# Optimization experiments

Measured on AMD Instinct MI355X. Metric: run time of the kernel, lower is better.

## Reference

```python
import jax, jax.numpy as jnp
import numpy as np

HEADS = 8


def setup_inputs() -> dict:
    key = jax.random.key(0)
    ks = jax.random.split(key, 9)
    B, C, W, H = 8, 512, 32, 32
    dk = C // HEADS
    return {
        "x": jax.random.normal(ks[0], (B, C, W, H), dtype=jnp.float32),
        "wq": jax.random.normal(ks[1], (C, C), dtype=jnp.float32) * (1.0 / np.sqrt(C)),
        "bq": jax.random.normal(ks[2], (C,), dtype=jnp.float32) * 0.02,
        "wk": jax.random.normal(ks[3], (C, C), dtype=jnp.float32) * (1.0 / np.sqrt(C)),
        "bk": jax.random.normal(ks[4], (C,), dtype=jnp.float32) * 0.02,
        "wv": jax.random.normal(ks[5], (C, C), dtype=jnp.float32) * (1.0 / np.sqrt(C)),
        "bv": jax.random.normal(ks[6], (C,), dtype=jnp.float32) * 0.02,
        "rel_h": jax.random.normal(ks[7], (1, HEADS, dk, 1, H), dtype=jnp.float32),
        "rel_w": jax.random.normal(ks[8], (1, HEADS, dk, W, 1), dtype=jnp.float32),
    }


def reference(x, wq, bq, wk, bk, wv, bv, rel_h, rel_w):
    B, C, W, H = x.shape
    dk = C // HEADS
    N = W * H

    def proj(w, b):
        # 1x1 conv == per-pixel linear map over channels
        y = jnp.einsum('bchw,oc->bohw', x, w) + b[None, :, None, None]
        return y.reshape(B, HEADS, dk, N)

    q = proj(wq, bq)  # [B, h, dk, N]
    k = proj(wk, bk)
    v = proj(wv, bv)

    # content-content: q^T k -> [B, h, N, N]
    content_content = jnp.einsum('bhdn,bhdm->bhnm', q, k)

    # content-position: (rel_h + rel_w) -> [1, h, dk, W, H] -> [h, dk, N]
    pos = (rel_h + rel_w).reshape(HEADS, dk, N)
    # matmul(pos^T, q): [h, N, dk] @ [B, h, dk, N] -> [B, h, N, N]
    content_position = jnp.einsum('hdn,bhdm->bhnm', pos, q)

    energy = content_content + content_position
    attention = jax.nn.softmax(energy, axis=-1)  # softmax over last dim

    # out = v @ attention^T : [B, h, dk, N]
    out = jnp.einsum('bhdn,bhmn->bhdm', v, attention)
    return out.reshape(B, C, W, H)
```

## Files before the change

kernel.cpp:

```cpp
#include <hip/hip_runtime.h>

#define NPIX 1024
#define CC   512
#define DK   64
#define LOG2E 1.4426950408889634f

typedef __attribute__((ext_vector_type(8)))  short s16x8;
typedef __attribute__((ext_vector_type(8)))  _Float16 f16x8;
typedef __attribute__((ext_vector_type(16))) float f32x16;

union U4 { uint4 u; s16x8 v; };
union U4H { uint4 u; f16x8 v; };

__device__ __forceinline__ ushort f2bf(float f) {
  uint u = __float_as_uint(f);
  uint r = (u + 0x7fffu + ((u >> 16) & 1u)) >> 16;
  return (ushort)r;
}
__device__ __forceinline__ float bf2f(ushort h) { return __uint_as_float(((uint)h) << 16); }
__device__ __forceinline__ ushort f2h(float f) {
  union { _Float16 h; ushort u; } c;
  c.h = (_Float16)f;
  return c.u;
}
__device__ __forceinline__ float h2f(ushort u) {
  union { ushort u; _Float16 h; } c;
  c.u = u;
  return (float)c.h;
}

__device__ __forceinline__ uint cvtpk(float a, float b) {
  uint r;
  asm("v_cvt_pk_bf16_f32 %0, %1, %2" : "=v"(r) : "v"(a), "v"(b));
  return r;
}
__device__ __forceinline__ float fmax3(float a, float b, float c) {
  float d;
  asm("v_max3_f32 %0, %1, %2, %3" : "=v"(d) : "v"(a), "v"(b), "v"(c));
  return d;
}
__device__ __forceinline__ float exp2raw(float x) {
  float r;
  asm("v_exp_f32 %0, %1" : "=v"(r) : "v"(x));
  return r;
}

__device__ __forceinline__ f32x16 mfma32(s16x8 a, s16x8 b, f32x16 c) {
  return __builtin_amdgcn_mfma_f32_32x32x16_bf16(a, b, c, 0, 0, 0);
}
__device__ __forceinline__ f32x16 mfma32h(f16x8 a, f16x8 b, f32x16 c) {
  return __builtin_amdgcn_mfma_f32_32x32x16_f16(a, b, c, 0, 0, 0);
}

__device__ __forceinline__ void gl16(const void* g, void* l) {
  __builtin_amdgcn_global_load_lds(
      (const __attribute__((address_space(1))) void*)g,
      (__attribute__((address_space(3))) void*)l, 16, 0, 0);
}

__global__ void pos_kernel(const float* __restrict__ rel_h,
                           const float* __restrict__ rel_w,
                           ushort* __restrict__ posH, ushort* __restrict__ posL) {
  int t = blockIdx.x * 256 + threadIdx.x;
  int g = t & 7;
  int n = (t >> 3) & (NPIX - 1);
  int h = t >> 13;
  int xw = n >> 5, yh = n & 31;
  ushort hbuf[8], lbuf[8];
#pragma unroll
  for (int j = 0; j < 8; ++j) {
    int d = g * 8 + j;
    float v = rel_h[(h * 64 + d) * 32 + yh] + rel_w[(h * 64 + d) * 32 + xw];
    ushort hi = f2h(v);
    hbuf[j] = hi;
    lbuf[j] = f2h(v - h2f(hi));
  }
  size_t base = ((size_t)(h * NPIX + n)) * 64 + g * 8;
  *(uint4*)&posH[base] = *(uint4*)hbuf;
  *(uint4*)&posL[base] = *(uint4*)lbuf;
}

__global__ __launch_bounds__(256) void cvt_w_kernel(
    const float* __restrict__ wq, const float* __restrict__ wk,
    const float* __restrict__ wv,
    ushort* __restrict__ Wh, ushort* __restrict__ Wl) {
  int lin8 = blockIdx.x * 256 + threadIdx.x;
  int p = lin8 >> 15;
  int o = (lin8 & 32767) >> 6;
  int co = lin8 & 63;
  const float* Wsrc = (p == 0) ? wq : (p == 1) ? wk : wv;
  const float* src = &Wsrc[o * CC + co * 8];
  float4 f0 = *(const float4*)src;
  float4 f1 = *(const float4*)(src + 4);
  float f[8] = {f0.x, f0.y, f0.z, f0.w, f1.x, f1.y, f1.z, f1.w};
  ushort h8[8], l8[8];
#pragma unroll
  for (int j = 0; j < 8; ++j) {
    float sv = f[j] * 64.0f;
    ushort hi = f2h(sv);
    h8[j] = hi;
    l8[j] = f2h(sv - h2f(hi));
  }
  size_t dst = ((size_t)(p * CC + o)) * CC + co * 8;
  *(uint4*)&Wh[dst] = *(uint4*)h8;
  *(uint4*)&Wl[dst] = *(uint4*)l8;
}

__global__ __launch_bounds__(256) void cvt_x_kernel(
    const float* __restrict__ x, ushort* __restrict__ Xh) {
  int t = blockIdx.x * 256 + threadIdx.x;
  int nl = t & (NPIX - 1);
  int rest = t >> 10;
  int co = rest & 63;
  int b = rest >> 6;
  ushort h8[8];
#pragma unroll
  for (int j = 0; j < 8; ++j) {
    float v = x[(((size_t)(b * CC + co * 8 + j)) << 10) + nl];
    h8[j] = f2h(v);
  }
  size_t dst = (((size_t)(b * NPIX + nl)) << 9) + co * 8;
  *(uint4*)&Xh[dst] = *(uint4*)h8;
}

__global__ __launch_bounds__(256, 2) void proj_kernel(
    const ushort* __restrict__ Xh, const ushort* __restrict__ Wh,
    const ushort* __restrict__ Wl,
    const float* __restrict__ bq, const float* __restrict__ bk,
    const float* __restrict__ bv,
    ushort* __restrict__ KQh, ushort* __restrict__ KQl,
    ushort* __restrict__ Vb) {
  __shared__ __align__(16) ushort sW[128 * 128];
  __shared__ __align__(16) ushort sX[128 * 64];

  int tid = threadIdx.x;
  int lane = tid & 63;
  int w = tid >> 6;
  int col = lane & 31;
  int half = lane >> 5;
  int srow = lane >> 4;
  int sslot = lane & 15;

  int z = blockIdx.z;
  int b = z / 3, p = z % 3;
  const float* bias = (p == 0) ? bq : (p == 1) ? bk : bv;

  int n0 = blockIdx.x * 128;
  int o0 = blockIdx.y * 128;
  int wo = w >> 1;
  int wn = w & 1;

  f32x16 acc[2][2];
#pragma unroll
  for (int i = 0; i < 2; ++i)
#pragma unroll
    for (int j = 0; j < 2; ++j)
#pragma unroll
      for (int r = 0; r < 16; ++r) acc[i][j][r] = 0.f;

#pragma unroll 1
  for (int c0 = 0; c0 < CC; c0 += 64) {
#pragma unroll
    for (int i = 0; i < 8; ++i) {
      int rbase = (i * 4 + w) * 4;
      int row = rbase + srow;
      int j = sslot ^ (row & 15);
      int jc = j & 7;
      const ushort* src = (j < 8 || p == 2) ? Wh : Wl;
      size_t g = ((size_t)(p * CC + o0 + row)) * CC + c0 + jc * 8;
      gl16(src + g, (char*)sW + rbase * 256);
    }
#pragma unroll
    for (int i = 0; i < 4; ++i) {
      int rbase = i * 32 + w * 8;
      int row = rbase + (lane >> 3);
      int jc = (lane & 7) ^ (row & 7);
      size_t g = ((size_t)(b * NPIX + n0 + row)) * CC + c0 + jc * 8;
      gl16(Xh + g, (char*)sX + rbase * 128);
    }
    __syncthreads();

#pragma unroll
    for (int s = 0; s < 4; ++s) {
      if (p < 2) {
        f16x8 xa[2], wh_[2], wl_[2];
#pragma unroll
        for (int mt = 0; mt < 2; ++mt) {
          int row = wn * 64 + mt * 32 + col;
          int slot = ((s * 2 + half) ^ (row & 7)) << 4;
          xa[mt] = *(const f16x8*)((const char*)sX + row * 128 + slot);
        }
#pragma unroll
        for (int ct = 0; ct < 2; ++ct) {
          int row = wo * 64 + ct * 32 + col;
          int sh = ((s * 2 + half) ^ (row & 15)) << 4;
          int sl = ((8 + s * 2 + half) ^ (row & 15)) << 4;
          wh_[ct] = *(const f16x8*)((const char*)sW + row * 256 + sh);
          wl_[ct] = *(const f16x8*)((const char*)sW + row * 256 + sl);
        }
#pragma unroll
        for (int mt = 0; mt < 2; ++mt)
#pragma unroll
          for (int ct = 0; ct < 2; ++ct) {
            acc[mt][ct] = mfma32h(xa[mt], wh_[ct], acc[mt][ct]);
            acc[mt][ct] = mfma32h(xa[mt], wl_[ct], acc[mt][ct]);
          }
      } else {
        f16x8 wa[2], xb[2];
#pragma unroll
        for (int mt = 0; mt < 2; ++mt) {
          int row = wo * 64 + mt * 32 + col;
          int sh = ((s * 2 + half) ^ (row & 15)) << 4;
          wa[mt] = *(const f16x8*)((const char*)sW + row * 256 + sh);
        }
#pragma unroll
        for (int ct = 0; ct < 2; ++ct) {
          int row = wn * 64 + ct * 32 + col;
          int slot = ((s * 2 + half) ^ (row & 7)) << 4;
          xb[ct] = *(const f16x8*)((const char*)sX + row * 128 + slot);
        }
#pragma unroll
        for (int mt = 0; mt < 2; ++mt)
#pragma unroll
          for (int ct = 0; ct < 2; ++ct)
            acc[mt][ct] = mfma32h(wa[mt], xb[ct], acc[mt][ct]);
      }
    }
    __syncthreads();
  }

  const float INV64 = 0.015625f;
  if (p < 2) {
    float qscale = (p == 0) ? LOG2E : 1.0f;
#pragma unroll
    for (int ct = 0; ct < 2; ++ct) {
      int o = o0 + wo * 64 + ct * 32 + col;
      int bh = b * 8 + (o >> 6);
      int kk = ((p == 0) ? 64 : 0) + (o & 63);
      float bias_v = bias[o];
#pragma unroll
      for (int mt = 0; mt < 2; ++mt) {
        int nbase = n0 + wn * 64 + mt * 32;
#pragma unroll
        for (int r = 0; r < 16; ++r) {
          int n = nbase + (r & 3) + 8 * (r >> 2) + 4 * half;
          float v = (acc[mt][ct][r] * INV64 + bias_v) * qscale;
          ushort hi = f2h(v);
          size_t addr = (((size_t)bh << 10) + n) * 128 + kk;
          KQh[addr] = hi;
          if (p == 0) KQl[addr] = f2h(v - h2f(hi));
        }
      }
    }
  } else {
#pragma unroll
    for (int ct = 0; ct < 2; ++ct) {
      int n = n0 + wn * 64 + ct * 32 + col;
#pragma unroll
      for (int mt = 0; mt < 2; ++mt) {
        int obase = o0 + wo * 64 + mt * 32;
#pragma unroll
        for (int r = 0; r < 16; ++r) {
          int o = obase + (r & 3) + 8 * (r >> 2) + 4 * half;
          int bh = b * 8 + (o >> 6);
          int d = o & 63;
          float v = acc[mt][ct][r] * INV64 + bias[o];
          Vb[(((size_t)(bh * 64 + d)) << 10) + n] = f2bf(v);
        }
      }
    }
  }
}

__global__ __launch_bounds__(256, 2) void attn_kernel(
    const ushort* __restrict__ KQh, const ushort* __restrict__ KQl,
    const ushort* __restrict__ posH, const ushort* __restrict__ posL,
    const ushort* __restrict__ Vb, float* __restrict__ out) {
  __shared__ __align__(16) ushort sKh[128 * 128];
  __shared__ __align__(16) ushort sV[64 * 128];

  int tid = threadIdx.x;
  int lane = tid & 63;
  int w = tid >> 6;

  int bid = blockIdx.x;
  int wg = (bid & 7) * 64 + (bid >> 3);
  int bh = wg >> 3;
  int qb = wg & 7;
  int h = bh & 7;

  int col = lane & 31;
  int half = lane >> 5;
  int q0 = qb * 128 + w * 32;
  int q = q0 + col;

  uint4 bqh[8], bql[8];
  {
    const ushort* rowQh = KQh + ((size_t)bh * NPIX + q) * 128;
    const ushort* rowQl = KQl + ((size_t)bh * NPIX + q) * 128;
#pragma unroll
    for (int s = 0; s < 4; ++s) {
      int off = 64 + s * 16 + half * 8;
      bqh[s] = *(const uint4*)(rowQh + off);
      bql[s] = *(const uint4*)(rowQl + off);
    }
    const ushort* rowPh = posH + ((size_t)(h * NPIX + q)) * 64;
    const ushort* rowPl = posL + ((size_t)(h * NPIX + q)) * 64;
#pragma unroll
    for (int s = 4; s < 8; ++s) {
      int off = (s - 4) * 16 + half * 8;
      bqh[s] = *(const uint4*)(rowPh + off);
      bql[s] = *(const uint4*)(rowPl + off);
    }
  }

  f32x16 oacc[2];
#pragma unroll
  for (int t = 0; t < 2; ++t)
#pragma unroll
    for (int r = 0; r < 16; ++r) oacc[t][r] = 0.f;
  float m_ = -1e30f, l_ = 0.f;

  int srow = lane >> 4;
  int sslot = lane & 15;

#pragma unroll 1
  for (int k0 = 0; k0 < NPIX; k0 += 128) {
#pragma unroll
    for (int i = 0; i < 8; ++i) {
      int row = w * 32 + i * 4 + srow;
      size_t goff = ((size_t)bh * NPIX + k0 + row) * 128 + ((sslot ^ (row & 15)) << 3);
      char* ldst = (char*)sKh + (w * 32 + i * 4) * 256;
      gl16(KQh + goff, ldst);
    }
#pragma unroll
    for (int i = 0; i < 4; ++i) {
      int d = w * 16 + i * 4 + srow;
      size_t goff = ((size_t)(bh * 64 + d)) * NPIX + k0 + ((sslot ^ (d & 15)) << 3);
      char* ldst = (char*)sV + (w * 16 + i * 4) * 256;
      gl16(Vb + goff, ldst);
    }
    __syncthreads();

    f32x16 sa[4];
#pragma unroll
    for (int t = 0; t < 4; ++t)
#pragma unroll
      for (int r = 0; r < 16; ++r) sa[t][r] = 0.f;

    __builtin_amdgcn_s_setprio(1);
#pragma unroll
    for (int s = 0; s < 8; ++s) {
      U4H ubh, ubl;
      ubh.u = bqh[s];
      ubl.u = bql[s];
#pragma unroll
      for (int t = 0; t < 4; ++t) {
        int row = t * 32 + col;
        int slot = ((s * 2 + half) ^ (row & 15)) << 4;
        const f16x8 ah = *(const f16x8*)((const char*)sKh + row * 256 + slot);
        sa[t] = mfma32h(ah, ubh.v, sa[t]);
        sa[t] = mfma32h(ah, ubl.v, sa[t]);
      }
    }
    __builtin_amdgcn_s_setprio(0);

    float mx = -1e30f;
#pragma unroll
    for (int t = 0; t < 4; ++t)
#pragma unroll
      for (int r = 0; r < 16; r += 2) mx = fmax3(mx, sa[t][r], sa[t][r + 1]);
    mx = fmaxf(mx, __shfl_xor(mx, 32));
    if (!__all(mx - m_ <= 11.54f)) {
      float mn = fmaxf(m_, mx);
      float sc = exp2raw(m_ - mn);
      l_ *= sc;
#pragma unroll
      for (int t = 0; t < 2; ++t)
#pragma unroll
        for (int r = 0; r < 16; ++r) oacc[t][r] *= sc;
      m_ = mn;
    }
    float ssum = 0.f;
#pragma unroll
    for (int t = 0; t < 4; ++t)
#pragma unroll
      for (int r = 0; r < 16; ++r) {
        float pv = exp2raw(sa[t][r] - m_);
        sa[t][r] = pv;
        ssum += pv;
      }
    ssum += __shfl_xor(ssum, 32);
    l_ += ssum;

#pragma unroll
    for (int t = 0; t < 4; ++t) {
      uint ua[4], ub[4], xa[4], xb[4];
#pragma unroll
      for (int g = 0; g < 4; ++g) {
        ua[g] = cvtpk(sa[t][4 * g + 0], sa[t][4 * g + 1]);
        ub[g] = cvtpk(sa[t][4 * g + 2], sa[t][4 * g + 3]);
      }
#pragma unroll
      for (int g = 0; g < 4; ++g) {
        xa[g] = __shfl_xor(ua[g], 32);
        xb[g] = __shfl_xor(ub[g], 32);
      }
      __builtin_amdgcn_s_setprio(1);
#pragma unroll
      for (int st = 0; st < 2; ++st) {
        int g = st * 2 + half;
        U4 pf;
        if (half == 0) {
          pf.u.x = ua[g]; pf.u.y = ub[g]; pf.u.z = xa[g]; pf.u.w = xb[g];
        } else {
          pf.u.x = xa[g]; pf.u.y = xb[g]; pf.u.z = ua[g]; pf.u.w = ub[g];
        }
#pragma unroll
        for (int dt = 0; dt < 2; ++dt) {
          int d = dt * 32 + col;
          int slot = ((t * 4 + st * 2 + half) ^ (d & 15)) << 4;
          const s16x8 vf = *(const s16x8*)((const char*)sV + d * 256 + slot);
          oacc[dt] = mfma32(vf, pf.v, oacc[dt]);
        }
      }
      __builtin_amdgcn_s_setprio(0);
    }
    __syncthreads();
  }

  float inv = 1.0f / l_;
#pragma unroll
  for (int dt = 0; dt < 2; ++dt)
#pragma unroll
    for (int r = 0; r < 16; ++r) {
      int d = dt * 32 + (r & 3) + 8 * (r >> 2) + 4 * half;
      out[((size_t)(bh * 64 + d) << 10) + q] = oacc[dt][r] * inv;
    }
}

extern "C" void kernel_launch(void* const* d_in, const int* in_sizes, int n_in,
                              void* d_out, int out_size, void* d_ws, size_t ws_size,
                              hipStream_t stream) {
  const float* x     = (const float*)d_in[0];
  const float* wq    = (const float*)d_in[1];
  const float* bq    = (const float*)d_in[2];
  const float* wk    = (const float*)d_in[3];
  const float* bk    = (const float*)d_in[4];
  const float* wv    = (const float*)d_in[5];
  const float* bv    = (const float*)d_in[6];
  const float* rel_h = (const float*)d_in[7];
  const float* rel_w = (const float*)d_in[8];
  float* out = (float*)d_out;

  const size_t MB = 1024 * 1024;
  char* ws = (char*)d_ws;
  ushort* KQh  = (ushort*)(ws);
  ushort* KQl  = (ushort*)(ws + 16 * MB);
  ushort* Vb   = (ushort*)(ws + 32 * MB);
  ushort* posH = (ushort*)(ws + 40 * MB);
  ushort* posL = (ushort*)(ws + 41 * MB);
  ushort* Xh   = (ushort*)(ws + 42 * MB);
  ushort* Wh   = (ushort*)(ws + 50 * MB);
  ushort* Wl   = (ushort*)(ws + 50 * MB + 1572864);

  pos_kernel<<<dim3(256), dim3(256), 0, stream>>>(rel_h, rel_w, posH, posL);
  cvt_w_kernel<<<dim3(384), dim3(256), 0, stream>>>(wq, wk, wv, Wh, Wl);
  cvt_x_kernel<<<dim3(2048), dim3(256), 0, stream>>>(x, Xh);
  proj_kernel<<<dim3(8, 4, 24), dim3(256), 0, stream>>>(
      Xh, Wh, Wl, bq, bk, bv, KQh, KQl, Vb);
  attn_kernel<<<dim3(512), dim3(256), 0, stream>>>(KQh, KQl, posH, posL, Vb, out);
}
```

Baseline: 108.7 us.

## Double-buffer K/V tiles in attention loop with 64-key chunks

Splits the key loop into 64-key chunks and double-buffers the K and V shared-memory tiles, issuing the next chunk's loads before computing on the current one, so global loads overlap with MFMA and softmax work. The V tile swizzle moves to an 8-slot pattern to fit the narrower rows. The max and sum reductions are rebalanced into trees to shorten dependency chains. Total LDS is unchanged, but with smaller chunks the online-softmax rescale check runs twice as often, and only one barrier per iteration guards the buffer reuse.

Result: no change. 109.1 us (+0.4%).

```diff
diff --git a/kernel.cpp b/kernel.cpp
--- a/kernel.cpp
+++ b/kernel.cpp
@@ -276,8 +276,8 @@
     const ushort* __restrict__ KQh, const ushort* __restrict__ KQl,
     const ushort* __restrict__ posH, const ushort* __restrict__ posL,
     const ushort* __restrict__ Vb, float* __restrict__ out) {
-  __shared__ __align__(16) ushort sKh[128 * 128];
-  __shared__ __align__(16) ushort sV[64 * 128];
+  __shared__ __align__(16) ushort sKh[2][64 * 128];
+  __shared__ __align__(16) ushort sV[2][64 * 64];
 
   int tid = threadIdx.x;
   int lane = tid & 63;
@@ -324,27 +324,35 @@
   int srow = lane >> 4;
   int sslot = lane & 15;
 
+#define STAGE(bufi, k0)                                                      \
+  {                                                                          \
+    _Pragma("unroll")                                                        \
+    for (int i = 0; i < 4; ++i) {                                            \
+      int row = w * 16 + i * 4 + srow;                                       \
+      size_t goff = ((size_t)bh * NPIX + (k0) + row) * 128 +                 \
+                    ((sslot ^ (row & 15)) << 3);                             \
+      gl16(KQh + goff, (char*)&sKh[bufi][0] + (w * 16 + i * 4) * 256);       \
+    }                                                                        \
+    _Pragma("unroll")                                                        \
+    for (int i = 0; i < 2; ++i) {                                            \
+      int d = w * 16 + i * 8 + (lane >> 3);                                  \
+      int ks = (lane & 7) ^ (d & 7);                                         \
+      size_t goff = ((size_t)(bh * 64 + d)) * NPIX + (k0) + (ks << 3);       \
+      gl16(Vb + goff, (char*)&sV[bufi][0] + (w * 16 + i * 8) * 128);         \
+    }                                                                        \
+  }
+
+  STAGE(0, 0);
+  __syncthreads();
+
 #pragma unroll 1
-  for (int k0 = 0; k0 < NPIX; k0 += 128) {
-#pragma unroll
-    for (int i = 0; i < 8; ++i) {
-      int row = w * 32 + i * 4 + srow;
-      size_t goff = ((size_t)bh * NPIX + k0 + row) * 128 + ((sslot ^ (row & 15)) << 3);
-      char* ldst = (char*)sKh + (w * 32 + i * 4) * 256;
-      gl16(KQh + goff, ldst);
-    }
-#pragma unroll
-    for (int i = 0; i < 4; ++i) {
-      int d = w * 16 + i * 4 + srow;
-      size_t goff = ((size_t)(bh * 64 + d)) * NPIX + k0 + ((sslot ^ (d & 15)) << 3);
-      char* ldst = (char*)sV + (w * 16 + i * 4) * 256;
-      gl16(Vb + goff, ldst);
-    }
-    __syncthreads();
-
-    f32x16 sa[4];
-#pragma unroll
-    for (int t = 0; t < 4; ++t)
+  for (int c = 0; c < 16; ++c) {
+    int buf = c & 1;
+    if (c < 15) STAGE(buf ^ 1, (c + 1) * 64);
+
+    f32x16 sa[2];
+#pragma unroll
+    for (int t = 0; t < 2; ++t)
 #pragma unroll
       for (int r = 0; r < 16; ++r) sa[t][r] = 0.f;
 
@@ -355,21 +363,27 @@
       ubh.u = bqh[s];
       ubl.u = bql[s];
 #pragma unroll
-      for (int t = 0; t < 4; ++t) {
+      for (int t = 0; t < 2; ++t) {
         int row = t * 32 + col;
         int slot = ((s * 2 + half) ^ (row & 15)) << 4;
-        const f16x8 ah = *(const f16x8*)((const char*)sKh + row * 256 + slot);
+        const f16x8 ah = *(const f16x8*)((const char*)&sKh[buf][0] + row * 256 + slot);
         sa[t] = mfma32h(ah, ubh.v, sa[t]);
         sa[t] = mfma32h(ah, ubl.v, sa[t]);
       }
     }
     __builtin_amdgcn_s_setprio(0);
 
-    float mx = -1e30f;
-#pragma unroll
-    for (int t = 0; t < 4; ++t)
-#pragma unroll
-      for (int r = 0; r < 16; r += 2) mx = fmax3(mx, sa[t][r], sa[t][r + 1]);
+    float mxp[4];
+#pragma unroll
+    for (int j = 0; j < 4; ++j) {
+      int ti = j >> 1;
+      int b0 = (j & 1) * 8;
+      float a = fmax3(sa[ti][b0 + 0], sa[ti][b0 + 1], sa[ti][b0 + 2]);
+      float b1 = fmax3(sa[ti][b0 + 3], sa[ti][b0 + 4], sa[ti][b0 + 5]);
+      float c1 = fmax3(sa[ti][b0 + 6], sa[ti][b0 + 7], a);
+      mxp[j] = fmaxf(b1, c1);
+    }
+    float mx = fmaxf(fmax3(mxp[0], mxp[1], mxp[2]), mxp[3]);
     mx = fmaxf(mx, __shfl_xor(mx, 32));
     if (!__all(mx - m_ <= 11.54f)) {
       float mn = fmaxf(m_, mx);
@@ -381,20 +395,23 @@
         for (int r = 0; r < 16; ++r) oacc[t][r] *= sc;
       m_ = mn;
     }
-    float ssum = 0.f;
-#pragma unroll
-    for (int t = 0; t < 4; ++t)
-#pragma unroll
-      for (int r = 0; r < 16; ++r) {
-        float pv = exp2raw(sa[t][r] - m_);
-        sa[t][r] = pv;
-        ssum += pv;
-      }
+#pragma unroll
+    for (int t = 0; t < 2; ++t)
+#pragma unroll
+      for (int r = 0; r < 16; ++r) sa[t][r] = exp2raw(sa[t][r] - m_);
+    float sp[8];
+#pragma unroll
+    for (int j = 0; j < 8; ++j) {
+      int ti = j >> 2;
+      int b0 = (j & 3) * 4;
+      sp[j] = (sa[ti][b0 + 0] + sa[ti][b0 + 1]) + (sa[ti][b0 + 2] + sa[ti][b0 + 3]);
+    }
+    float ssum = ((sp[0] + sp[1]) + (sp[2] + sp[3])) + ((sp[4] + sp[5]) + (sp[6] + sp[7]));
     ssum += __shfl_xor(ssum, 32);
     l_ += ssum;
 
 #pragma unroll
-    for (int t = 0; t < 4; ++t) {
+    for (int t = 0; t < 2; ++t) {
       uint ua[4], ub[4], xa[4], xb[4];
 #pragma unroll
       for (int g = 0; g < 4; ++g) {
@@ -419,8 +436,8 @@
 #pragma unroll
         for (int dt = 0; dt < 2; ++dt) {
           int d = dt * 32 + col;
-          int slot = ((t * 4 + st * 2 + half) ^ (d & 15)) << 4;
-          const s16x8 vf = *(const s16x8*)((const char*)sV + d * 256 + slot);
+          int slot = ((t * 4 + st * 2 + half) ^ (d & 7)) << 4;
+          const s16x8 vf = *(const s16x8*)((const char*)&sV[buf][0] + d * 128 + slot);
           oacc[dt] = mfma32(vf, pf.v, oacc[dt]);
         }
       }
@@ -428,6 +445,7 @@
     }
     __syncthreads();
   }
+#undef STAGE
 
   float inv = 1.0f / l_;
 #pragma unroll
```
